# Kernel tuning notes

Hardware: AMD Instinct MI355X
Metric: run time of the kernel (lower is better)

The kernel has to match this reference:

```python
import jax, jax.numpy as jnp
import numpy as np


def setup_inputs() -> dict:
    key = jax.random.key(0)
    ks = jax.random.split(key, 5)
    B, H, W, C, R = 4, 64, 64, 256, 32
    x = jax.random.normal(ks[0], (B, H, W, C), dtype=jnp.float32)
    # 1x1 conv kernels stored as [C_in, C_out] matrices (equivalent math)
    w_f = jax.random.normal(ks[1], (C, R), dtype=jnp.float32) * (1.0 / np.sqrt(C))
    w_g = jax.random.normal(ks[2], (C, R), dtype=jnp.float32) * (1.0 / np.sqrt(C))
    w_h = jax.random.normal(ks[3], (C, R), dtype=jnp.float32) * (1.0 / np.sqrt(C))
    w_v = jax.random.normal(ks[4], (R, C), dtype=jnp.float32) * (1.0 / np.sqrt(R))
    gamma = jnp.zeros((1,), dtype=jnp.float32)
    return {"x": x, "w_f": w_f, "w_g": w_g, "w_h": w_h, "w_v": w_v, "gamma": gamma}


def reference(x, w_f, w_g, w_h, w_v, gamma):
    B, H, W, C = x.shape
    N = H * W
    xt = x.reshape(B, N, C)                       # flatten spatial tokens
    f = jnp.einsum('bnc,cr->bnr', xt, w_f)        # 1x1 conv == token-wise matmul
    g = jnp.einsum('bnc,cr->bnr', xt, w_g)
    h = jnp.einsum('bnc,cr->bnr', xt, w_h)
    scores = jnp.einsum('bnr,bmr->bnm', f, g)     # [B, N, N]
    # NOTE: original softmaxes over axis=1 (the query/row axis), not axis=-1
    attn = jax.nn.softmax(scores, axis=1)
    y = jnp.einsum('bnm,bmr->bnr', attn, h)       # [B, N, R]
    y = jnp.einsum('bnr,rc->bnc', y, w_v)         # output 1x1 conv
    y = y.reshape(B, H, W, C)
    return gamma * y + x
```

## Files before the change

kernel.cpp:

```cpp
#include <hip/hip_runtime.h>


#define BB 4
#define NN 4096
#define CC 256
#define RR 32
#define CSEG 4
#define MP 40
#define LOG2E 1.44269504088896340736f

typedef short short8 __attribute__((ext_vector_type(8)));
typedef unsigned short ushort8 __attribute__((ext_vector_type(8)));
typedef float floatx4 __attribute__((ext_vector_type(4)));

#define MFMA16 __builtin_amdgcn_mfma_f32_16x16x32_bf16

static __device__ __forceinline__ unsigned short f2bf(float f) {
  union { float f; unsigned u; } v; v.f = f;
  const unsigned r = v.u + 0x7fffu + ((v.u >> 16) & 1u);
  return (unsigned short)(r >> 16);
}
static __device__ __forceinline__ unsigned bfpack(float lo, float hi) {
  return __builtin_amdgcn_perm(__float_as_uint(hi), __float_as_uint(lo), 0x07060302u);
}

__global__ __launch_bounds__(256) void k_prep(
    const float* __restrict__ wf, const float* __restrict__ wg,
    const float* __restrict__ wh, const float* __restrict__ wv,
    unsigned short* __restrict__ wfrag, unsigned short* __restrict__ wvfrag) {
  const int idx = blockIdx.x * 256 + threadIdx.x;
  const int lane = (idx >> 3) & 63;
  const int j = idx & 7;
  const int col = lane & 15, q = lane >> 4;
  if (idx < 24576) {
    const int mat = idx >> 13;
    const int fid = (idx >> 9) & 15;
    const int kc = fid >> 1, nt = fid & 1;
    const float* w = (mat == 0) ? wf : ((mat == 1) ? wg : wh);
    wfrag[idx] = f2bf(w[(kc * 32 + q * 8 + j) * RR + nt * 16 + col]);
  } else {
    const int r = idx - 24576;
    const int t = (r >> 9) & 15;
    wvfrag[r] = f2bf(wv[(q * 8 + j) * CC + t * 16 + col]);
  }
}

__global__ __launch_bounds__(256) void k_fgh(
    const float* __restrict__ x, const unsigned short* __restrict__ wfrag,
    unsigned short* __restrict__ f16, unsigned short* __restrict__ g16,
    unsigned short* __restrict__ hT16) {
  __shared__ unsigned short wflds[24576];
  const int tid = threadIdx.x, lane = tid & 63, wave = tid >> 6;
  const int col = lane & 15, q = lane >> 4;
  {
    const uint4* src = (const uint4*)wfrag;
    uint4* dst = (uint4*)wflds;
#pragma unroll
    for (int i = 0; i < 12; ++i) dst[tid + i * 256] = src[tid + i * 256];
  }
  __syncthreads();
  const int t0 = blockIdx.x * 64 + wave * 16;
  short8 af[8];
  const float* xr = x + (long)(t0 + col) * CC + q * 8;
#pragma unroll
  for (int kc = 0; kc < 8; ++kc) {
    float tmp[8];
    *(float4*)(tmp) = *(const float4*)(xr + kc * 32);
    *(float4*)(tmp + 4) = *(const float4*)(xr + kc * 32 + 4);
    short8 o;
#pragma unroll
    for (int j = 0; j < 8; ++j) o[j] = (short)f2bf(tmp[j]);
    af[kc] = o;
  }
  const floatx4 zero = {0.f, 0.f, 0.f, 0.f};
  floatx4 acc[3][2];
#pragma unroll
  for (int m = 0; m < 3; ++m) { acc[m][0] = zero; acc[m][1] = zero; }
#pragma unroll
  for (int kc = 0; kc < 8; ++kc) {
#pragma unroll
    for (int mat = 0; mat < 3; ++mat) {
#pragma unroll
      for (int nt = 0; nt < 2; ++nt) {
        const short8 bf = *(const short8*)(wflds + (mat * 16 + kc * 2 + nt) * 512 + lane * 8);
        acc[mat][nt] = MFMA16(af[kc], bf, acc[mat][nt], 0, 0, 0);
      }
    }
  }
  const int b = t0 >> 12;
#pragma unroll
  for (int nt = 0; nt < 2; ++nt) {
#pragma unroll
    for (int r = 0; r < 4; ++r) {
      const int tok = t0 + q * 4 + r;
      const int n = nt * 16 + col;
      f16[(long)tok * RR + n] = f2bf(acc[0][nt][r] * LOG2E);
      g16[(long)tok * RR + n] = f2bf(acc[1][nt][r]);
      hT16[((long)b * RR + n) * NN + (tok & (NN - 1))] = f2bf(acc[2][nt][r]);
    }
  }
}

__global__ __launch_bounds__(256) void k_colsum(
    const unsigned short* __restrict__ f16, const unsigned short* __restrict__ g16,
    float* __restrict__ psum) {
  const int tid = threadIdx.x, lane = tid & 63, wave = tid >> 6;
  const int col = lane & 15, q = lane >> 4;
  const int mblk = blockIdx.x & 31;
  const int b = (blockIdx.x >> 5) & 3;
  const int seg = blockIdx.x >> 7;
  const int m0 = mblk * 128 + wave * 32;
  const short8 bg1 = *(const short8*)(g16 + ((long)(b * NN + m0 + col)) * RR + q * 8);
  const short8 bg2 = *(const short8*)(g16 + ((long)(b * NN + m0 + 16 + col)) * RR + q * 8);
  const floatx4 zero = {0.f, 0.f, 0.f, 0.f};
  float s1 = 0.f, s2 = 0.f;
  const unsigned short* fb = f16 + ((long)b * NN + seg * (NN / CSEG)) * RR;
#pragma unroll 4
  for (int n = 0; n < NN / CSEG; n += 16) {
    const short8 af = *(const short8*)(fb + (long)(n + col) * RR + q * 8);
    const floatx4 d1 = MFMA16(af, bg1, zero, 0, 0, 0);
    const floatx4 d2 = MFMA16(af, bg2, zero, 0, 0, 0);
    s1 += __builtin_amdgcn_exp2f(d1[0]) + __builtin_amdgcn_exp2f(d1[1]) +
          __builtin_amdgcn_exp2f(d1[2]) + __builtin_amdgcn_exp2f(d1[3]);
    s2 += __builtin_amdgcn_exp2f(d2[0]) + __builtin_amdgcn_exp2f(d2[1]) +
          __builtin_amdgcn_exp2f(d2[2]) + __builtin_amdgcn_exp2f(d2[3]);
  }
  s1 += __shfl_xor(s1, 16); s1 += __shfl_xor(s1, 32);
  s2 += __shfl_xor(s2, 16); s2 += __shfl_xor(s2, 32);
  if (lane < 16) {
    psum[(long)seg * (BB * NN) + b * NN + m0 + lane] = s1;
    psum[(long)seg * (BB * NN) + b * NN + m0 + 16 + lane] = s2;
  }
}

__global__ __launch_bounds__(256) void k_scaleh(
    const float* __restrict__ psum, unsigned short* __restrict__ hT16) {
  const long i8 = ((long)blockIdx.x * 256 + threadIdx.x) * 8;
  const int b = (int)(i8 >> 17);
  const int m = (int)(i8 & (NN - 1));
  float cs[8] = {0.f, 0.f, 0.f, 0.f, 0.f, 0.f, 0.f, 0.f};
#pragma unroll
  for (int sg = 0; sg < CSEG; ++sg) {
    const float* p = psum + (long)sg * (BB * NN) + b * NN + m;
    const float4 a = *(const float4*)p;
    const float4 c = *(const float4*)(p + 4);
    cs[0] += a.x; cs[1] += a.y; cs[2] += a.z; cs[3] += a.w;
    cs[4] += c.x; cs[5] += c.y; cs[6] += c.z; cs[7] += c.w;
  }
  const ushort8 hv = *(const ushort8*)(hT16 + i8);
  ushort8 o;
#pragma unroll
  for (int j = 0; j < 8; ++j) {
    const float h = __uint_as_float(((unsigned)hv[j]) << 16);
    o[j] = f2bf(h * __builtin_amdgcn_rcpf(cs[j]));
  }
  *(ushort8*)(hT16 + i8) = o;
}

#define C_ADDR(TN, TM) (((TN) + col) * MP + (TM) + q * 4)
__global__ __launch_bounds__(256, 4) void k_pvout(
    const unsigned short* __restrict__ f16, const unsigned short* __restrict__ g16,
    const unsigned short* __restrict__ hT16, const unsigned short* __restrict__ wvfrag,
    const float* __restrict__ x, const float* __restrict__ gamma,
    float* __restrict__ out) {
  __shared__ float ylds[4][32 * 36];
  __shared__ unsigned short pt_all[4][32 * MP];
  const int tid = threadIdx.x, lane = tid & 63, wave = tid >> 6;
  const int col = lane & 15, q = lane >> 4;
  const int b = blockIdx.x >> 7;
  const int t0 = (blockIdx.x & 127) * 32;
  const floatx4 zero = {0.f, 0.f, 0.f, 0.f};
  const short8 af1 = *(const short8*)(f16 + ((long)(b * NN + t0 + col)) * RR + q * 8);
  const short8 af2 = *(const short8*)(f16 + ((long)(b * NN + t0 + 16 + col)) * RR + q * 8);
  floatx4 a11 = zero, a12 = zero, a21 = zero, a22 = zero;
  unsigned short* pt = &pt_all[wave][0];
  const unsigned short* gb = g16 + (long)b * NN * RR;
  const unsigned short* hb = hT16 + (long)b * RR * NN;
  const int mq = wave * 1024;
#pragma unroll 2
  for (int mi = 0; mi < 1024; mi += 32) {
    const int m0 = mq + mi;
    const short8 bg1 = *(const short8*)(gb + (long)(m0 + col) * RR + q * 8);
    const short8 bg2 = *(const short8*)(gb + (long)(m0 + 16 + col) * RR + q * 8);
    const floatx4 d00 = MFMA16(bg1, af1, zero, 0, 0, 0);
    const floatx4 d01 = MFMA16(bg2, af1, zero, 0, 0, 0);
    const floatx4 d10 = MFMA16(bg1, af2, zero, 0, 0, 0);
    const floatx4 d11 = MFMA16(bg2, af2, zero, 0, 0, 0);
    float w0, w1, w2, w3;
    w0 = __builtin_amdgcn_exp2f(d00[0]); w1 = __builtin_amdgcn_exp2f(d00[1]);
    w2 = __builtin_amdgcn_exp2f(d00[2]); w3 = __builtin_amdgcn_exp2f(d00[3]);
    *(uint2*)(pt + C_ADDR(0, 0)) = make_uint2(bfpack(w0, w1), bfpack(w2, w3));
    w0 = __builtin_amdgcn_exp2f(d01[0]); w1 = __builtin_amdgcn_exp2f(d01[1]);
    w2 = __builtin_amdgcn_exp2f(d01[2]); w3 = __builtin_amdgcn_exp2f(d01[3]);
    *(uint2*)(pt + C_ADDR(0, 16)) = make_uint2(bfpack(w0, w1), bfpack(w2, w3));
    w0 = __builtin_amdgcn_exp2f(d10[0]); w1 = __builtin_amdgcn_exp2f(d10[1]);
    w2 = __builtin_amdgcn_exp2f(d10[2]); w3 = __builtin_amdgcn_exp2f(d10[3]);
    *(uint2*)(pt + C_ADDR(16, 0)) = make_uint2(bfpack(w0, w1), bfpack(w2, w3));
    w0 = __builtin_amdgcn_exp2f(d11[0]); w1 = __builtin_amdgcn_exp2f(d11[1]);
    w2 = __builtin_amdgcn_exp2f(d11[2]); w3 = __builtin_amdgcn_exp2f(d11[3]);
    *(uint2*)(pt + C_ADDR(16, 16)) = make_uint2(bfpack(w0, w1), bfpack(w2, w3));
    const short8 ap1 = *(const short8*)(pt + col * MP + q * 8);
    const short8 ap2 = *(const short8*)(pt + (col + 16) * MP + q * 8);
    const short8 bh1 = *(const short8*)(hb + (long)col * NN + m0 + q * 8);
    const short8 bh2 = *(const short8*)(hb + (long)(col + 16) * NN + m0 + q * 8);
    a11 = MFMA16(ap1, bh1, a11, 0, 0, 0);
    a12 = MFMA16(ap1, bh2, a12, 0, 0, 0);
    a21 = MFMA16(ap2, bh1, a21, 0, 0, 0);
    a22 = MFMA16(ap2, bh2, a22, 0, 0, 0);
  }
  {
    float* yp = &ylds[wave][0];
#pragma unroll
    for (int r = 0; r < 4; ++r) {
      yp[(q * 4 + r) * 36 + col] = a11[r];
      yp[(q * 4 + r) * 36 + col + 16] = a12[r];
      yp[(16 + q * 4 + r) * 36 + col] = a21[r];
      yp[(16 + q * 4 + r) * 36 + col + 16] = a22[r];
    }
  }
  __syncthreads();
  {
    const int tile = wave & 1, hh = wave >> 1;
    float s[8] = {0.f, 0.f, 0.f, 0.f, 0.f, 0.f, 0.f, 0.f};
#pragma unroll
    for (int w2 = 0; w2 < 4; ++w2) {
      const float* yp = &ylds[w2][(tile * 16 + col) * 36 + q * 8];
      const float4 u0 = *(const float4*)yp;
      const float4 u1 = *(const float4*)(yp + 4);
      s[0] += u0.x; s[1] += u0.y; s[2] += u0.z; s[3] += u0.w;
      s[4] += u1.x; s[5] += u1.y; s[6] += u1.z; s[7] += u1.w;
    }
    short8 ay;
#pragma unroll
    for (int j = 0; j < 8; ++j) ay[j] = (short)f2bf(s[j]);
    const float gm = gamma[0];
    float* sc = (float*)pt;
    const int row = lane >> 2, c4 = (lane & 3) * 4;
#pragma unroll
    for (int tp = 0; tp < 8; tp += 2) {
      const short8 bw0 = *(const short8*)(wvfrag + (hh * 8 + tp) * 512 + lane * 8);
      const short8 bw1 = *(const short8*)(wvfrag + (hh * 8 + tp + 1) * 512 + lane * 8);
      const floatx4 d0 = MFMA16(ay, bw0, zero, 0, 0, 0);
      const floatx4 d1 = MFMA16(ay, bw1, zero, 0, 0, 0);
#pragma unroll
      for (int r = 0; r < 4; ++r) {
        sc[(q * 4 + r) * 36 + col] = d0[r];
        sc[(q * 4 + r) * 36 + col + 16] = d1[r];
      }
#pragma unroll
      for (int j = 0; j < 2; ++j) {
        const float4 v = *(const float4*)(sc + row * 36 + c4 + j * 16);
        const long gidx = (long)(b * NN + t0 + tile * 16 + row) * CC +
                          hh * 128 + tp * 16 + j * 16 + c4;
        const float4 xv = *(const float4*)(x + gidx);
        float4 o;
        o.x = gm * v.x + xv.x; o.y = gm * v.y + xv.y;
        o.z = gm * v.z + xv.z; o.w = gm * v.w + xv.w;
        *(float4*)(out + gidx) = o;
      }
    }
  }
}

extern "C" void kernel_launch(void* const* d_in, const int* in_sizes, int n_in,
                              void* d_out, int out_size, void* d_ws, size_t ws_size,
                              hipStream_t stream) {
  const float* x = (const float*)d_in[0];
  const float* wf = (const float*)d_in[1];
  const float* wg = (const float*)d_in[2];
  const float* wh = (const float*)d_in[3];
  const float* wv = (const float*)d_in[4];
  const float* gamma = (const float*)d_in[5];
  float* out = (float*)d_out;

  unsigned short* f16 = (unsigned short*)d_ws;
  unsigned short* g16 = f16 + (long)BB * NN * RR;
  unsigned short* hT16 = g16 + (long)BB * NN * RR;
  unsigned short* wfrag = hT16 + (long)BB * NN * RR;
  unsigned short* wvfrag = wfrag + 24576;
  float* psum = (float*)(wvfrag + 8192);

  k_prep<<<128, 256, 0, stream>>>(wf, wg, wh, wv, wfrag, wvfrag);
  k_fgh<<<BB * NN / 64, 256, 0, stream>>>(x, wfrag, f16, g16, hT16);
  k_colsum<<<CSEG * BB * 32, 256, 0, stream>>>(f16, g16, psum);
  k_scaleh<<<BB * RR * NN / 2048, 256, 0, stream>>>(psum, hT16);
  k_pvout<<<BB * 128, 256, 0, stream>>>(f16, g16, hT16, wvfrag, x, gamma, out);
}
```

Baseline: 124.3 us.

## Fold softmax column normalization into PV kernel via log-sum MFMA bias

Removes the separate kernel that rescaled the bf16 transposed h by the reciprocal column sums. Instead, each PV block sums the partial column sums into shared memory as -log2(sum). It then uses those values as the MFMA accumulator init, so exp2 directly yields normalized attention weights. This drops one kernel launch and a read-modify-write pass over h. In exchange, every block redundantly reads all column partial sums for its batch and needs 16KB more LDS plus a block barrier, which may lower occupancy.

```diff
diff --git a/kernel.cpp b/kernel.cpp
--- a/kernel.cpp
+++ b/kernel.cpp
@@ -133,43 +133,26 @@
   }
 }
 
-__global__ __launch_bounds__(256) void k_scaleh(
-    const float* __restrict__ psum, unsigned short* __restrict__ hT16) {
-  const long i8 = ((long)blockIdx.x * 256 + threadIdx.x) * 8;
-  const int b = (int)(i8 >> 17);
-  const int m = (int)(i8 & (NN - 1));
-  float cs[8] = {0.f, 0.f, 0.f, 0.f, 0.f, 0.f, 0.f, 0.f};
-#pragma unroll
-  for (int sg = 0; sg < CSEG; ++sg) {
-    const float* p = psum + (long)sg * (BB * NN) + b * NN + m;
-    const float4 a = *(const float4*)p;
-    const float4 c = *(const float4*)(p + 4);
-    cs[0] += a.x; cs[1] += a.y; cs[2] += a.z; cs[3] += a.w;
-    cs[4] += c.x; cs[5] += c.y; cs[6] += c.z; cs[7] += c.w;
-  }
-  const ushort8 hv = *(const ushort8*)(hT16 + i8);
-  ushort8 o;
-#pragma unroll
-  for (int j = 0; j < 8; ++j) {
-    const float h = __uint_as_float(((unsigned)hv[j]) << 16);
-    o[j] = f2bf(h * __builtin_amdgcn_rcpf(cs[j]));
-  }
-  *(ushort8*)(hT16 + i8) = o;
-}
-
 #define C_ADDR(TN, TM) (((TN) + col) * MP + (TM) + q * 4)
 __global__ __launch_bounds__(256, 4) void k_pvout(
     const unsigned short* __restrict__ f16, const unsigned short* __restrict__ g16,
     const unsigned short* __restrict__ hT16, const unsigned short* __restrict__ wvfrag,
-    const float* __restrict__ x, const float* __restrict__ gamma,
-    float* __restrict__ out) {
+    const float* __restrict__ psum, const float* __restrict__ x,
+    const float* __restrict__ gamma, float* __restrict__ out) {
   __shared__ float ylds[4][32 * 36];
   __shared__ unsigned short pt_all[4][32 * MP];
+  __shared__ float lcis[NN];
   const int tid = threadIdx.x, lane = tid & 63, wave = tid >> 6;
   const int col = lane & 15, q = lane >> 4;
   const int b = blockIdx.x >> 7;
   const int t0 = (blockIdx.x & 127) * 32;
   const floatx4 zero = {0.f, 0.f, 0.f, 0.f};
+  for (int i = tid; i < NN; i += 256) {
+    float s = 0.f;
+#pragma unroll
+    for (int sg = 0; sg < CSEG; ++sg) s += psum[(long)sg * (BB * NN) + b * NN + i];
+    lcis[i] = -__builtin_amdgcn_logf(s);
+  }
   const short8 af1 = *(const short8*)(f16 + ((long)(b * NN + t0 + col)) * RR + q * 8);
   const short8 af2 = *(const short8*)(f16 + ((long)(b * NN + t0 + 16 + col)) * RR + q * 8);
   floatx4 a11 = zero, a12 = zero, a21 = zero, a22 = zero;
@@ -177,15 +160,18 @@
   const unsigned short* gb = g16 + (long)b * NN * RR;
   const unsigned short* hb = hT16 + (long)b * RR * NN;
   const int mq = wave * 1024;
+  __syncthreads();
 #pragma unroll 2
   for (int mi = 0; mi < 1024; mi += 32) {
     const int m0 = mq + mi;
     const short8 bg1 = *(const short8*)(gb + (long)(m0 + col) * RR + q * 8);
     const short8 bg2 = *(const short8*)(gb + (long)(m0 + 16 + col) * RR + q * 8);
-    const floatx4 d00 = MFMA16(bg1, af1, zero, 0, 0, 0);
-    const floatx4 d01 = MFMA16(bg2, af1, zero, 0, 0, 0);
-    const floatx4 d10 = MFMA16(bg1, af2, zero, 0, 0, 0);
-    const floatx4 d11 = MFMA16(bg2, af2, zero, 0, 0, 0);
+    const floatx4 cia = *(const floatx4*)(lcis + m0 + q * 4);
+    const floatx4 cib = *(const floatx4*)(lcis + m0 + 16 + q * 4);
+    const floatx4 d00 = MFMA16(bg1, af1, cia, 0, 0, 0);
+    const floatx4 d01 = MFMA16(bg2, af1, cib, 0, 0, 0);
+    const floatx4 d10 = MFMA16(bg1, af2, cia, 0, 0, 0);
+    const floatx4 d11 = MFMA16(bg2, af2, cib, 0, 0, 0);
     float w0, w1, w2, w3;
     w0 = __builtin_amdgcn_exp2f(d00[0]); w1 = __builtin_amdgcn_exp2f(d00[1]);
     w2 = __builtin_amdgcn_exp2f(d00[2]); w3 = __builtin_amdgcn_exp2f(d00[3]);
@@ -283,6 +269,5 @@
   k_prep<<<128, 256, 0, stream>>>(wf, wg, wh, wv, wfrag, wvfrag);
   k_fgh<<<BB * NN / 64, 256, 0, stream>>>(x, wfrag, f16, g16, hT16);
   k_colsum<<<CSEG * BB * 32, 256, 0, stream>>>(f16, g16, psum);
-  k_scaleh<<<BB * RR * NN / 2048, 256, 0, stream>>>(psum, hT16);
-  k_pvout<<<BB * 128, 256, 0, stream>>>(f16, g16, hT16, wvfrag, x, gamma, out);
-}
+  k_pvout<<<BB * 128, 256, 0, stream>>>(f16, g16, hT16, wvfrag, psum, x, gamma, out);
+}
```

Result: no change. 126.4 us (+1.7%).
